# Performance work log

Measured on AMD Instinct MI355X. Metric: run time of the kernel, lower is better.

The kernel has to match this reference:

```python
import jax, jax.numpy as jnp
import numpy as np

NUM_CLASSES = 1000
FEAT_DIM = 128
BATCH = 1_000_000


def setup_inputs() -> dict:
    key = jax.random.key(0)
    k1, k2, k3 = jax.random.split(key, 3)
    x = jax.random.normal(k1, (BATCH, FEAT_DIM), dtype=jnp.float32)
    labels = jax.random.randint(k2, (BATCH,), 0, NUM_CLASSES, dtype=jnp.int32)
    centers = jax.random.normal(k3, (NUM_CLASSES, FEAT_DIM), dtype=jnp.float32)
    return {"x": x, "labels": labels, "centers": centers}


def reference(x, labels, centers):
    # margin = ||centers[0] - centers[1]|| / 10, computed from detached centers at init
    margin = jax.lax.stop_gradient(jnp.sqrt(jnp.sum((centers[0] - centers[1]) ** 2)) / 10.0)
    # gather the center for each sample: (N, d)
    cb = centers[labels]
    # per-sample squared euclidean distance == diag of the original's N x N addmm matrix
    d = jnp.sum(x * x, axis=1) + jnp.sum(cb * cb, axis=1) - 2.0 * jnp.sum(x * cb, axis=1)
    hinge = jnp.maximum(jnp.float32(0.0), d - margin)
    batch_size = x.shape[0]
    return jnp.sum(hinge) / (batch_size * 2 * 2)
```

## Files before the change

kernel.cpp:

```cpp
#include <hip/hip_runtime.h>
#include <math.h>

#define N_BATCH 1000000
#define FEAT 128
#define FEAT4 32
#define GRID_MAIN 2048
#define BLOCK_MAIN 256
#define GROUPS_PER_BLOCK 8

__global__ void nh_precompute(const float* __restrict__ centers,
                              double* __restrict__ acc,
                              float* __restrict__ margin_out) {
    int lane = threadIdx.x;
    float s = 0.0f;
    for (int k = lane; k < FEAT; k += 64) {
        float d = centers[k] - centers[FEAT + k];
        s += d * d;
    }
    #pragma unroll
    for (int m = 32; m >= 1; m >>= 1) s += __shfl_xor(s, m);
    if (lane == 0) {
        *acc = 0.0;
        *margin_out = sqrtf(s) * 0.1f;
    }
}

__global__ __launch_bounds__(BLOCK_MAIN)
void nh_main(const float4* __restrict__ x,
             const int* __restrict__ labels,
             const float4* __restrict__ centers,
             const float* __restrict__ margin_p,
             double* __restrict__ acc) {
    const float margin = *margin_p;
    const int lane32 = threadIdx.x & 31;
    const int group  = threadIdx.x >> 5;
    const int stride = GRID_MAIN * GROUPS_PER_BLOCK;

    float local = 0.0f;
    for (int row = blockIdx.x * GROUPS_PER_BLOCK + group; row < N_BATCH; row += stride) {
        const int lbl = labels[row];
        const float4 xv = x[(size_t)row * FEAT4 + lane32];
        const float4 cv = centers[(size_t)lbl * FEAT4 + lane32];
        float dx = xv.x - cv.x;
        float s  = dx * dx;
        dx = xv.y - cv.y; s = fmaf(dx, dx, s);
        dx = xv.z - cv.z; s = fmaf(dx, dx, s);
        dx = xv.w - cv.w; s = fmaf(dx, dx, s);
        s += __shfl_xor(s, 16);
        s += __shfl_xor(s, 8);
        s += __shfl_xor(s, 4);
        s += __shfl_xor(s, 2);
        s += __shfl_xor(s, 1);
        if (lane32 == 0) {
            float h = s - margin;
            local += (h > 0.0f) ? h : 0.0f;
        }
    }

    #pragma unroll
    for (int m = 32; m >= 1; m >>= 1) local += __shfl_xor(local, m);
    __shared__ float wavesum[BLOCK_MAIN / 64];
    const int wid = threadIdx.x >> 6;
    if ((threadIdx.x & 63) == 0) wavesum[wid] = local;
    __syncthreads();
    if (threadIdx.x == 0) {
        float t = 0.0f;
        #pragma unroll
        for (int w = 0; w < BLOCK_MAIN / 64; ++w) t += wavesum[w];
        atomicAdd(acc, (double)t);
    }
}

__global__ void nh_finalize(const double* __restrict__ acc, float* __restrict__ out) {
    out[0] = (float)(*acc * (1.0 / ((double)N_BATCH * 4.0)));
}

extern "C" void kernel_launch(void* const* d_in, const int* in_sizes, int n_in,
                              void* d_out, int out_size, void* d_ws, size_t ws_size,
                              hipStream_t stream) {
    const float* x       = (const float*)d_in[0];
    const int*   labels  = (const int*)d_in[1];
    const float* centers = (const float*)d_in[2];
    float* out = (float*)d_out;

    double* acc    = (double*)d_ws;
    float*  margin = (float*)((char*)d_ws + 8);

    nh_precompute<<<1, 64, 0, stream>>>(centers, acc, margin);
    nh_main<<<GRID_MAIN, BLOCK_MAIN, 0, stream>>>(
        (const float4*)x, labels, (const float4*)centers, margin, acc);
    nh_finalize<<<1, 1, 0, stream>>>(acc, out);
}
```

Baseline: 660.4 us.

## Unroll row loop by two and replace double atomics with per-block partials

The main grid-stride loop now handles two rows per iteration, issuing both rows' label, x and center loads before the math. This raises memory-level parallelism per wave, and the two shuffle reductions are interleaved. The 2048 double-precision atomic adds are replaced by per-block float partials that a 256-thread finalize kernel reduces, which removes atomic contention. Register use per thread goes up, and the final sum is now in float rather than double.

```diff
diff --git a/kernel.cpp b/kernel.cpp
--- a/kernel.cpp
+++ b/kernel.cpp
@@ -7,9 +7,10 @@
 #define GRID_MAIN 2048
 #define BLOCK_MAIN 256
 #define GROUPS_PER_BLOCK 8
+#define ROW_STRIDE (GRID_MAIN * GROUPS_PER_BLOCK)
+
 
 __global__ void nh_precompute(const float* __restrict__ centers,
-                              double* __restrict__ acc,
                               float* __restrict__ margin_out) {
     int lane = threadIdx.x;
     float s = 0.0f;
@@ -20,7 +21,6 @@
     #pragma unroll
     for (int m = 32; m >= 1; m >>= 1) s += __shfl_xor(s, m);
     if (lane == 0) {
-        *acc = 0.0;
         *margin_out = sqrtf(s) * 0.1f;
     }
 }
@@ -30,30 +30,54 @@
              const int* __restrict__ labels,
              const float4* __restrict__ centers,
              const float* __restrict__ margin_p,
-             double* __restrict__ acc) {
+             float* __restrict__ partials) {
     const float margin = *margin_p;
     const int lane32 = threadIdx.x & 31;
     const int group  = threadIdx.x >> 5;
-    const int stride = GRID_MAIN * GROUPS_PER_BLOCK;
 
     float local = 0.0f;
-    for (int row = blockIdx.x * GROUPS_PER_BLOCK + group; row < N_BATCH; row += stride) {
-        const int lbl = labels[row];
-        const float4 xv = x[(size_t)row * FEAT4 + lane32];
-        const float4 cv = centers[(size_t)lbl * FEAT4 + lane32];
-        float dx = xv.x - cv.x;
-        float s  = dx * dx;
-        dx = xv.y - cv.y; s = fmaf(dx, dx, s);
-        dx = xv.z - cv.z; s = fmaf(dx, dx, s);
-        dx = xv.w - cv.w; s = fmaf(dx, dx, s);
-        s += __shfl_xor(s, 16);
-        s += __shfl_xor(s, 8);
-        s += __shfl_xor(s, 4);
-        s += __shfl_xor(s, 2);
-        s += __shfl_xor(s, 1);
+    int row = blockIdx.x * GROUPS_PER_BLOCK + group;
+
+    for (; row + ROW_STRIDE < N_BATCH; row += 2 * ROW_STRIDE) {
+        const int r1 = row + ROW_STRIDE;
+        const int l0 = labels[row];
+        const int l1 = labels[r1];
+        const float4 xv0 = x[(size_t)row * FEAT4 + lane32];
+        const float4 xv1 = x[(size_t)r1  * FEAT4 + lane32];
+        const float4 cv0 = centers[(size_t)l0 * FEAT4 + lane32];
+        const float4 cv1 = centers[(size_t)l1 * FEAT4 + lane32];
+
+        float d0 = xv0.x - cv0.x; float s0 = d0 * d0;
+        float d1 = xv1.x - cv1.x; float s1 = d1 * d1;
+        d0 = xv0.y - cv0.y; s0 = fmaf(d0, d0, s0);
+        d1 = xv1.y - cv1.y; s1 = fmaf(d1, d1, s1);
+        d0 = xv0.z - cv0.z; s0 = fmaf(d0, d0, s0);
+        d1 = xv1.z - cv1.z; s1 = fmaf(d1, d1, s1);
+        d0 = xv0.w - cv0.w; s0 = fmaf(d0, d0, s0);
+        d1 = xv1.w - cv1.w; s1 = fmaf(d1, d1, s1);
+
+        #pragma unroll
+        for (int m = 16; m >= 1; m >>= 1) {
+            s0 += __shfl_xor(s0, m);
+            s1 += __shfl_xor(s1, m);
+        }
         if (lane32 == 0) {
-            float h = s - margin;
-            local += (h > 0.0f) ? h : 0.0f;
+            float h0 = s0 - margin; local += (h0 > 0.0f) ? h0 : 0.0f;
+            float h1 = s1 - margin; local += (h1 > 0.0f) ? h1 : 0.0f;
+        }
+    }
+    if (row < N_BATCH) {
+        const int l0 = labels[row];
+        const float4 xv0 = x[(size_t)row * FEAT4 + lane32];
+        const float4 cv0 = centers[(size_t)l0 * FEAT4 + lane32];
+        float d0 = xv0.x - cv0.x; float s0 = d0 * d0;
+        d0 = xv0.y - cv0.y; s0 = fmaf(d0, d0, s0);
+        d0 = xv0.z - cv0.z; s0 = fmaf(d0, d0, s0);
+        d0 = xv0.w - cv0.w; s0 = fmaf(d0, d0, s0);
+        #pragma unroll
+        for (int m = 16; m >= 1; m >>= 1) s0 += __shfl_xor(s0, m);
+        if (lane32 == 0) {
+            float h0 = s0 - margin; local += (h0 > 0.0f) ? h0 : 0.0f;
         }
     }
 
@@ -67,12 +91,24 @@
         float t = 0.0f;
         #pragma unroll
         for (int w = 0; w < BLOCK_MAIN / 64; ++w) t += wavesum[w];
-        atomicAdd(acc, (double)t);
+        partials[blockIdx.x] = t;
     }
 }
 
-__global__ void nh_finalize(const double* __restrict__ acc, float* __restrict__ out) {
-    out[0] = (float)(*acc * (1.0 / ((double)N_BATCH * 4.0)));
+__global__ __launch_bounds__(256)
+void nh_finalize(const float* __restrict__ partials, float* __restrict__ out) {
+    float s = 0.0f;
+    for (int i = threadIdx.x; i < GRID_MAIN; i += 256) s += partials[i];
+    #pragma unroll
+    for (int m = 32; m >= 1; m >>= 1) s += __shfl_xor(s, m);
+    __shared__ float wavesum[4];
+    const int wid = threadIdx.x >> 6;
+    if ((threadIdx.x & 63) == 0) wavesum[wid] = s;
+    __syncthreads();
+    if (threadIdx.x == 0) {
+        float t = wavesum[0] + wavesum[1] + wavesum[2] + wavesum[3];
+        out[0] = t * (1.0f / ((float)N_BATCH * 4.0f));
+    }
 }
 
 extern "C" void kernel_launch(void* const* d_in, const int* in_sizes, int n_in,
@@ -83,11 +119,11 @@
     const float* centers = (const float*)d_in[2];
     float* out = (float*)d_out;
 
-    double* acc    = (double*)d_ws;
-    float*  margin = (float*)((char*)d_ws + 8);
+    float* margin   = (float*)d_ws;
+    float* partials = (float*)((char*)d_ws + 16);
 
-    nh_precompute<<<1, 64, 0, stream>>>(centers, acc, margin);
+    nh_precompute<<<1, 64, 0, stream>>>(centers, margin);
     nh_main<<<GRID_MAIN, BLOCK_MAIN, 0, stream>>>(
-        (const float4*)x, labels, (const float4*)centers, margin, acc);
-    nh_finalize<<<1, 1, 0, stream>>>(acc, out);
+        (const float4*)x, labels, (const float4*)centers, margin, partials);
+    nh_finalize<<<1, 256, 0, stream>>>(partials, out);
 }
```

Result: no change. 655.1 us (-0.8%).
